# Performance work log

Measured on AMD Instinct MI355X. Metric: run time of the kernel, lower is better.

## Reference

```python
import jax, jax.numpy as jnp
import numpy as np

N = 50000
E = 800000
IN_C = 128
HID = 64
HEADS = 4
NUM_CLASSES = 10
NUM_GRAPHS = 64
EPS = 1e-5
NEG_SLOPE = 0.2


def setup_inputs() -> dict:
    key = jax.random.key(0)
    ks = jax.random.split(key, 32)
    inp = {}
    inp["x"] = jax.random.normal(ks[0], (N, IN_C), dtype=jnp.float32)
    inp["edge_index"] = jax.random.randint(ks[1], (2, E), 0, N, dtype=jnp.int32)
    inp["batch"] = jnp.sort(jax.random.randint(ks[2], (N,), 0, NUM_GRAPHS, dtype=jnp.int32))
    s = 0.05
    # GATConv1: in=128 -> heads=4, hid=64, concat -> 256
    inp["W1"] = jax.random.normal(ks[3], (IN_C, HEADS * HID), dtype=jnp.float32) * s
    inp["a_src1"] = jax.random.normal(ks[4], (HEADS, HID), dtype=jnp.float32) * s
    inp["a_dst1"] = jax.random.normal(ks[5], (HEADS, HID), dtype=jnp.float32) * s
    inp["b1"] = jnp.zeros((HEADS * HID,), dtype=jnp.float32)
    inp["g1"] = jnp.ones((HEADS * HID,), dtype=jnp.float32)
    inp["be1"] = jnp.zeros((HEADS * HID,), dtype=jnp.float32)
    # GATConv2: in=256 -> heads=4, hid=64, concat -> 256
    inp["W2"] = jax.random.normal(ks[6], (HEADS * HID, HEADS * HID), dtype=jnp.float32) * s
    inp["a_src2"] = jax.random.normal(ks[7], (HEADS, HID), dtype=jnp.float32) * s
    inp["a_dst2"] = jax.random.normal(ks[8], (HEADS, HID), dtype=jnp.float32) * s
    inp["b2"] = jnp.zeros((HEADS * HID,), dtype=jnp.float32)
    inp["g2"] = jnp.ones((HEADS * HID,), dtype=jnp.float32)
    inp["be2"] = jnp.zeros((HEADS * HID,), dtype=jnp.float32)
    # GATConv3: in=256 -> heads=1, hid=64, mean (concat=False) -> 64
    inp["W3"] = jax.random.normal(ks[9], (HEADS * HID, 1 * HID), dtype=jnp.float32) * s
    inp["a_src3"] = jax.random.normal(ks[10], (1, HID), dtype=jnp.float32) * s
    inp["a_dst3"] = jax.random.normal(ks[11], (1, HID), dtype=jnp.float32) * s
    inp["b3"] = jnp.zeros((HID,), dtype=jnp.float32)
    inp["g3"] = jnp.ones((HID,), dtype=jnp.float32)
    inp["be3"] = jnp.zeros((HID,), dtype=jnp.float32)
    # final classifier
    inp["fcW"] = jax.random.normal(ks[12], (HID, NUM_CLASSES), dtype=jnp.float32) * s
    inp["fcb"] = jnp.zeros((NUM_CLASSES,), dtype=jnp.float32)
    return inp


def gat_conv(x, src, dst, W, a_src, a_dst, b, heads, out_c, concat):
    # Linear transform, split heads: [N, H, C]
    h = (x @ W).reshape(-1, heads, out_c)
    # Per-node attention logits (dot with per-head attention vectors): [N, H]
    as_ = jnp.einsum("nhc,hc->nh", h, a_src)
    ad_ = jnp.einsum("nhc,hc->nh", h, a_dst)
    # Per-edge unnormalized attention (src contributes a_src, dst a_dst)
    e = jax.nn.leaky_relu(as_[src] + ad_[dst], NEG_SLOPE)  # [E, H]
    # Segment softmax over destination node (stable)
    e_max = jax.ops.segment_max(e, dst, num_segments=N)  # [N, H]
    ex = jnp.exp(e - e_max[dst])
    denom = jax.ops.segment_sum(ex, dst, num_segments=N)  # [N, H]
    alpha = ex / denom[dst]  # [E, H]
    # Weighted scatter-aggregate of source features
    msg = h[src] * alpha[:, :, None]  # [E, H, C]
    out = jax.ops.segment_sum(msg, dst, num_segments=N)  # [N, H, C]
    out = out.reshape(-1, heads * out_c) if concat else out.mean(axis=1)
    return out + b


def batch_norm(x, gamma, beta):
    mean = x.mean(axis=0)
    var = x.var(axis=0)
    return (x - mean) * jax.lax.rsqrt(var + EPS) * gamma + beta


def reference(x, edge_index, batch, W1, a_src1, a_dst1, b1, g1, be1,
              W2, a_src2, a_dst2, b2, g2, be2,
              W3, a_src3, a_dst3, b3, g3, be3, fcW, fcb):
    src, dst = edge_index[0], edge_index[1]
    h = jax.nn.relu(gat_conv(x, src, dst, W1, a_src1, a_dst1, b1, HEADS, HID, True))
    h = batch_norm(h, g1, be1)  # dropout = identity (eval)
    h = jax.nn.relu(gat_conv(h, src, dst, W2, a_src2, a_dst2, b2, HEADS, HID, True))
    h = batch_norm(h, g2, be2)
    h = jax.nn.relu(gat_conv(h, src, dst, W3, a_src3, a_dst3, b3, 1, HID, False))
    h = batch_norm(h, g3, be3)
    # global mean pool over graphs
    sums = jax.ops.segment_sum(h, batch, num_segments=NUM_GRAPHS)  # [G, HID]
    counts = jax.ops.segment_sum(jnp.ones((h.shape[0],), h.dtype), batch, num_segments=NUM_GRAPHS)
    pooled = sums / jnp.maximum(counts, 1.0)[:, None]
    return pooled @ fcW + fcb
```

## Files before the change

kernel.cpp:

```cpp
#include <hip/hip_runtime.h>
#include <hip/hip_bf16.h>

#define N_NODES 50000
#define NUM_E   800000
#define EPS_BN  1e-5f
#define NUM_GRAPHS 64

typedef __attribute__((ext_vector_type(8))) short bf16x8;
typedef __attribute__((ext_vector_type(4))) float f32x4;
typedef unsigned short ushort_t;
typedef unsigned int uint_t;

static __device__ __forceinline__ unsigned short f2bf(float f) {
    unsigned int u = __float_as_uint(f);
    u += 0x7fffu + ((u >> 16) & 1u);
    return (unsigned short)(u >> 16);
}
static __device__ __forceinline__ uint_t pkbf(float lo, float hi) {
    __hip_bfloat162 t = __float22bfloat162_rn(make_float2(lo, hi));
    return *(uint_t*)&t;
}
static __device__ __forceinline__ float bflo(uint_t u) { return __uint_as_float(u << 16); }
static __device__ __forceinline__ float bfhi(uint_t u) { return __uint_as_float(u & 0xffff0000u); }

__global__ void hist_kernel(const int* __restrict__ ei, int* __restrict__ deg) {
    int e = blockIdx.x * blockDim.x + threadIdx.x;
    if (e >= NUM_E) return;
    atomicAdd(&deg[ei[NUM_E + e]], 1);
}

__global__ void scan_local_kernel(const int* __restrict__ deg, int* __restrict__ rowptr,
                                  int* __restrict__ bsum) {
    __shared__ int ws[4];
    int b = blockIdx.x, t = threadIdx.x;
    int i = b * 256 + t;
    int lane = t & 63, wv = t >> 6;
    int v = (i < N_NODES) ? deg[i] : 0;
    int incl = v;
#pragma unroll
    for (int off = 1; off < 64; off <<= 1) {
        int u = __shfl_up(incl, off, 64);
        if (lane >= off) incl += u;
    }
    if (lane == 63) ws[wv] = incl;
    __syncthreads();
    if (t == 0) {
        int s = 0;
#pragma unroll
        for (int k = 0; k < 4; ++k) { int x = ws[k]; ws[k] = s; s += x; }
        bsum[b] = s;
    }
    __syncthreads();
    if (i < N_NODES) rowptr[i + 1] = ws[wv] + incl;
}

__global__ void scan_sums_kernel(int* __restrict__ bsum, int nb) {
    __shared__ int ws[4];
    int t = threadIdx.x;
    int lane = t & 63, wv = t >> 6;
    int v = (t < nb) ? bsum[t] : 0;
    int incl = v;
#pragma unroll
    for (int off = 1; off < 64; off <<= 1) {
        int u = __shfl_up(incl, off, 64);
        if (lane >= off) incl += u;
    }
    if (lane == 63) ws[wv] = incl;
    __syncthreads();
    if (t == 0) {
        int s = 0;
#pragma unroll
        for (int k = 0; k < 4; ++k) { int x = ws[k]; ws[k] = s; s += x; }
    }
    __syncthreads();
    if (t < nb) bsum[t] = ws[wv] + incl - v;
}

__global__ void scan_add_kernel(int* __restrict__ rowptr, const int* __restrict__ bsum) {
    int b = blockIdx.x, t = threadIdx.x;
    int i = b * 256 + t;
    if (i < N_NODES) rowptr[i + 1] += bsum[b];
    if (b == 0 && t == 0) rowptr[0] = 0;
}

__global__ void scatter_kernel(const int* __restrict__ ei, const int* __restrict__ rowptr,
                               int* __restrict__ fill, int* __restrict__ srcs) {
    int e = blockIdx.x * blockDim.x + threadIdx.x;
    if (e >= NUM_E) return;
    int dst = ei[NUM_E + e];
    int pos = rowptr[dst] + atomicAdd(&fill[dst], 1);
    srcs[pos] = ei[e];
}

__global__ void batch_offsets_kernel(const int* __restrict__ batch, int* __restrict__ goff) {
    int g = threadIdx.x;
    if (g > NUM_GRAPHS) return;
    int lo = 0, hi = N_NODES;
    while (lo < hi) {
        int mid = (lo + hi) >> 1;
        if (batch[mid] < g) lo = mid + 1; else hi = mid;
    }
    goff[g] = lo;
}

__global__ void prep_all_kernel(const float* __restrict__ W1, const float* __restrict__ W2,
                                const float* __restrict__ W3, const float* __restrict__ x,
                                ushort_t* __restrict__ w1t, ushort_t* __restrict__ w2t,
                                ushort_t* __restrict__ w3t, ushort_t* __restrict__ xbf) {
    const int S1 = 128 * 256, S2 = 256 * 256, S3 = 256 * 64;
    const int SW = S1 + S2 + S3;
    const int SX = N_NODES * 128 / 4;
    int i = blockIdx.x * blockDim.x + threadIdx.x;
    if (i < SX) {
        float4 v = ((const float4*)x)[i];
        ((uint2*)xbf)[i] = make_uint2(pkbf(v.x, v.y), pkbf(v.z, v.w));
    } else if (i < SX + SW) {
        int j = i - SX;
        if (j < S1) {
            int k = j / 256, n = j % 256;
            w1t[n * 128 + k] = f2bf(W1[j]);
        } else if (j < S1 + S2) {
            int jj = j - S1; int k = jj / 256, n = jj % 256;
            w2t[n * 256 + k] = f2bf(W2[jj]);
        } else {
            int jj = j - S1 - S2; int k = jj / 64, n = jj % 64;
            w3t[n * 256 + k] = f2bf(W3[jj]);
        }
    }
}

template<int K, int NFULL, int BN>
__global__ __launch_bounds__(256) void gemm_fused_kernel(const ushort_t* __restrict__ A,
                                                         const ushort_t* __restrict__ Bt,
                                                         ushort_t* __restrict__ C,
                                                         const float* __restrict__ stats,
                                                         const float* __restrict__ g,
                                                         const float* __restrict__ be,
                                                         const float* __restrict__ a_src,
                                                         const float* __restrict__ a_dst,
                                                         float* __restrict__ as_,
                                                         float* __restrict__ ad_) {
    const int NT = BN / 16;
    const int NG = BN / 64;
    constexpr int LOOP_BYTES = (128 * 40 + BN * 40) * 2;
    constexpr int EPI_BYTES  = 4 * 32 * 64 * 2;
    constexpr int SMEM_BYTES = LOOP_BYTES > EPI_BYTES ? LOOP_BYTES : EPI_BYTES;
    __shared__ __align__(16) unsigned char smem[SMEM_BYTES];
    ushort_t (*As)[40]     = (ushort_t (*)[40])smem;
    ushort_t (*Bs)[40]     = (ushort_t (*)[40])(smem + 128 * 40 * 2);
    ushort_t (*Cs)[32][64] = (ushort_t (*)[32][64])smem;
    __shared__ __align__(16) float aff_a[K], aff_b[K];
    __shared__ float asrc_s[BN], adst_s[BN];
    int tid = threadIdx.x;
    int lane = tid & 63, w = tid >> 6;
    int row0 = blockIdx.x * 128, col0 = blockIdx.y * BN;
    int m_l = lane & 15, q = lane >> 4;

    for (int c = tid; c < K; c += 256) {
        float a = 1.f, b = 0.f;
        if (stats) {
            float m = stats[c] * (1.f / N_NODES);
            float var = fmaxf(stats[256 + c] * (1.f / N_NODES) - m * m, 0.f);
            float rs = rsqrtf(var + EPS_BN) * g[c];
            a = rs; b = be[c] - m * rs;
        }
        aff_a[c] = a; aff_b[c] = b;
    }
    if (tid < BN) {
        asrc_s[tid] = a_src[col0 + tid];
        adst_s[tid] = a_dst[col0 + tid];
    }
    __syncthreads();

    f32x4 acc[2][NT];
#pragma unroll
    for (int r = 0; r < 2; ++r)
#pragma unroll
        for (int c = 0; c < NT; ++c) acc[r][c] = (f32x4){0.f, 0.f, 0.f, 0.f};

    int ar = tid >> 1, ako = (tid & 1) * 16;

    for (int k0 = 0; k0 < K; k0 += 32) {
        uint_t ow[8];
        int gr = row0 + ar;
        uint4 u0 = make_uint4(0, 0, 0, 0), u1 = make_uint4(0, 0, 0, 0);
        if (gr < N_NODES) {
            const ushort_t* ap = A + (long)gr * K + k0 + ako;
            u0 = *(const uint4*)ap;
            u1 = *(const uint4*)(ap + 8);
        }
        uint_t uu[8] = {u0.x, u0.y, u0.z, u0.w, u1.x, u1.y, u1.z, u1.w};
#pragma unroll
        for (int t = 0; t < 8; ++t) {
            int k = k0 + ako + t * 2;
            float lo = bflo(uu[t]) * aff_a[k] + aff_b[k];
            float hi = bfhi(uu[t]) * aff_a[k + 1] + aff_b[k + 1];
            ow[t] = pkbf(lo, hi);
        }
        if constexpr (BN == 128) {
            int br = tid >> 1, bko = (tid & 1) * 16;
            const ushort_t* bp = Bt + (long)(col0 + br) * K + k0 + bko;
            uint4 b0 = *(const uint4*)bp;
            uint4 b1 = *(const uint4*)(bp + 8);
            *(uint4*)&As[ar][ako] = make_uint4(ow[0], ow[1], ow[2], ow[3]);
            *(uint4*)&As[ar][ako + 8] = make_uint4(ow[4], ow[5], ow[6], ow[7]);
            *(uint4*)&Bs[br][bko] = b0;
            *(uint4*)&Bs[br][bko + 8] = b1;
        } else {
            int br = tid >> 2, bko = (tid & 3) * 8;
            uint4 bv = *(const uint4*)(Bt + (long)(col0 + br) * K + k0 + bko);
            *(uint4*)&As[ar][ako] = make_uint4(ow[0], ow[1], ow[2], ow[3]);
            *(uint4*)&As[ar][ako + 8] = make_uint4(ow[4], ow[5], ow[6], ow[7]);
            *(uint4*)&Bs[br][bko] = bv;
        }
        __syncthreads();

        bf16x8 af[2];
#pragma unroll
        for (int r = 0; r < 2; ++r)
            af[r] = *(const bf16x8*)&As[w * 32 + r * 16 + m_l][q * 8];
#pragma unroll
        for (int c = 0; c < NT; ++c) {
            bf16x8 bf = *(const bf16x8*)&Bs[c * 16 + m_l][q * 8];
#pragma unroll
            for (int r = 0; r < 2; ++r)
                acc[r][c] = __builtin_amdgcn_mfma_f32_16x16x32_bf16(af[r], bf, acc[r][c], 0, 0, 0);
        }
        __syncthreads();
    }

    const int H = NFULL / 64;
#pragma unroll
    for (int gblk = 0; gblk < NG; ++gblk) {
        int hidx = blockIdx.y * NG + gblk;
        int colg = col0 + gblk * 64;
#pragma unroll
        for (int r = 0; r < 2; ++r)
#pragma unroll
            for (int cc = 0; cc < 4; ++cc)
#pragma unroll
                for (int i = 0; i < 4; ++i)
                    Cs[w][r * 16 + q * 4 + i][cc * 16 + m_l] = f2bf(acc[r][gblk * 4 + cc][i]);
#pragma unroll
        for (int j = 0; j < 4; ++j) {
            int flat = j * 64 + lane;
            int lr = flat >> 3, chg = flat & 7;
            int gr = row0 + w * 32 + lr;
            uint4 u = *(uint4*)&Cs[w][lr][chg * 8];
            float f0 = bflo(u.x), f1 = bfhi(u.x), f2 = bflo(u.y), f3 = bfhi(u.y);
            float f4 = bflo(u.z), f5 = bfhi(u.z), f6 = bflo(u.w), f7 = bfhi(u.w);
            int cb = gblk * 64 + chg * 8;
            float s1 = f0 * asrc_s[cb] + f1 * asrc_s[cb + 1] + f2 * asrc_s[cb + 2] + f3 * asrc_s[cb + 3]
                     + f4 * asrc_s[cb + 4] + f5 * asrc_s[cb + 5] + f6 * asrc_s[cb + 6] + f7 * asrc_s[cb + 7];
            float s2 = f0 * adst_s[cb] + f1 * adst_s[cb + 1] + f2 * adst_s[cb + 2] + f3 * adst_s[cb + 3]
                     + f4 * adst_s[cb + 4] + f5 * adst_s[cb + 5] + f6 * adst_s[cb + 6] + f7 * adst_s[cb + 7];
#pragma unroll
            for (int o = 1; o < 8; o <<= 1) {
                s1 += __shfl_xor(s1, o, 64);
                s2 += __shfl_xor(s2, o, 64);
            }
            if (gr < N_NODES) {
                *(uint4*)(C + (long)gr * NFULL + colg + chg * 8) = u;
                if ((lane & 7) == 0) {
                    as_[gr * H + hidx] = s1;
                    ad_[gr * H + hidx] = s2;
                }
            }
        }
    }
}

__global__ __launch_bounds__(256) void agg4_kernel(const ushort_t* __restrict__ h,
                                                   const float* __restrict__ as_,
                                                   const float* __restrict__ ad_,
                                                   const int* __restrict__ rowptr,
                                                   const int* __restrict__ srcs,
                                                   const float* __restrict__ bias,
                                                   ushort_t* __restrict__ out) {
    __shared__ float4 alf[4][4][17];
    __shared__ int    sed[4][4][17];
    int tid = threadIdx.x;
    int lane = tid & 63, w = tid >> 6;
    int q = lane >> 4, cl = lane & 15;
    int n = blockIdx.x * 16 + w * 4 + q;

    int start = rowptr[n];
    int deg = rowptr[n + 1] - start;

    float4 adv = *(const float4*)(ad_ + n * 4);
    float ad4[4] = {adv.x, adv.y, adv.z, adv.w};

    float mx[4] = {-1e30f, -1e30f, -1e30f, -1e30f};
    float dn[4] = {0.f, 0.f, 0.f, 0.f};
    {
        float vst[4] = {-1e30f, -1e30f, -1e30f, -1e30f};
        int s0 = 0;
        if (deg > 0) s0 = srcs[start + min(cl, deg - 1)];
        sed[w][q][cl] = s0;
        if (cl < deg) {
            float4 av = *(const float4*)(as_ + s0 * 4);
            float vv[4] = {av.x + ad4[0], av.y + ad4[1], av.z + ad4[2], av.w + ad4[3]};
#pragma unroll
            for (int hh = 0; hh < 4; ++hh) {
                float v = vv[hh] > 0.f ? vv[hh] : 0.2f * vv[hh];
                vst[hh] = v; mx[hh] = v; dn[hh] = 1.f;
            }
        }
        alf[w][q][cl] = make_float4(vst[0], vst[1], vst[2], vst[3]);
        for (int j = cl + 16; j < deg; j += 16) {
            int s = srcs[start + j];
            float4 av = *(const float4*)(as_ + s * 4);
            float vv[4] = {av.x + ad4[0], av.y + ad4[1], av.z + ad4[2], av.w + ad4[3]};
#pragma unroll
            for (int hh = 0; hh < 4; ++hh) {
                float v = vv[hh] > 0.f ? vv[hh] : 0.2f * vv[hh];
                float mn = fmaxf(mx[hh], v);
                dn[hh] = dn[hh] * __expf(mx[hh] - mn) + __expf(v - mn);
                mx[hh] = mn;
            }
        }
    }
    float mloc[4] = {mx[0], mx[1], mx[2], mx[3]};
#pragma unroll
    for (int off = 1; off < 16; off <<= 1)
#pragma unroll
        for (int hh = 0; hh < 4; ++hh) mx[hh] = fmaxf(mx[hh], __shfl_xor(mx[hh], off, 64));
#pragma unroll
    for (int hh = 0; hh < 4; ++hh) dn[hh] *= __expf(mloc[hh] - mx[hh]);
#pragma unroll
    for (int off = 1; off < 16; off <<= 1)
#pragma unroll
        for (int hh = 0; hh < 4; ++hh) dn[hh] += __shfl_xor(dn[hh], off, 64);
    float inv[4];
#pragma unroll
    for (int hh = 0; hh < 4; ++hh) inv[hh] = dn[hh] > 0.f ? 1.f / dn[hh] : 0.f;
    {
        float4 vv = alf[w][q][cl];
        alf[w][q][cl] = make_float4(__expf(vv.x - mx[0]) * inv[0], __expf(vv.y - mx[1]) * inv[1],
                                    __expf(vv.z - mx[2]) * inv[2], __expf(vv.w - mx[3]) * inv[3]);
    }

    int hd = cl >> 2, cbase = cl * 16;
    float acc[16];
#pragma unroll
    for (int k = 0; k < 16; ++k) acc[k] = 0.f;

    for (int chunk = 0; chunk < deg || chunk == 0; chunk += 16) {
        if (chunk > 0) {
            int j = chunk + cl;
            int s = srcs[start + min(j, deg - 1)];
            sed[w][q][cl] = s;
            float a4[4] = {0.f, 0.f, 0.f, 0.f};
            if (j < deg) {
                float4 av = *(const float4*)(as_ + s * 4);
                float vv[4] = {av.x + ad4[0], av.y + ad4[1], av.z + ad4[2], av.w + ad4[3]};
#pragma unroll
                for (int hh = 0; hh < 4; ++hh) {
                    float v = vv[hh] > 0.f ? vv[hh] : 0.2f * vv[hh];
                    a4[hh] = __expf(v - mx[hh]) * inv[hh];
                }
            }
            alf[w][q][cl] = make_float4(a4[0], a4[1], a4[2], a4[3]);
        }
        int cnt = min(16, deg - chunk);
        if (cnt < 0) cnt = 0;
        int e = 0;
        for (; e + 4 <= cnt; e += 4) {
            float av[4]; int sv[4];
#pragma unroll
            for (int t = 0; t < 4; ++t) {
                av[t] = ((const float*)&alf[w][q][e + t])[hd];
                sv[t] = sed[w][q][e + t];
            }
            uint4 ua[4];
#pragma unroll
            for (int t = 0; t < 4; ++t)
                ua[t] = *(const uint4*)(h + (long)sv[t] * 256 + cbase);
#pragma unroll
            for (int t = 0; t < 4; ++t) {
                float al = av[t];
                acc[0] += al * bflo(ua[t].x); acc[1] += al * bfhi(ua[t].x);
                acc[2] += al * bflo(ua[t].y); acc[3] += al * bfhi(ua[t].y);
                acc[4] += al * bflo(ua[t].z); acc[5] += al * bfhi(ua[t].z);
                acc[6] += al * bflo(ua[t].w); acc[7] += al * bfhi(ua[t].w);
            }
#pragma unroll
            for (int t = 0; t < 4; ++t)
                ua[t] = *(const uint4*)(h + (long)sv[t] * 256 + cbase + 8);
#pragma unroll
            for (int t = 0; t < 4; ++t) {
                float al = av[t];
                acc[8]  += al * bflo(ua[t].x); acc[9]  += al * bfhi(ua[t].x);
                acc[10] += al * bflo(ua[t].y); acc[11] += al * bfhi(ua[t].y);
                acc[12] += al * bflo(ua[t].z); acc[13] += al * bfhi(ua[t].z);
                acc[14] += al * bflo(ua[t].w); acc[15] += al * bfhi(ua[t].w);
            }
        }
        for (; e < cnt; ++e) {
            float al = ((const float*)&alf[w][q][e])[hd];
            const ushort_t* hr = h + (long)sed[w][q][e] * 256 + cbase;
            uint4 u0 = *(const uint4*)hr;
            uint4 u1 = *(const uint4*)(hr + 8);
            acc[0]  += al * bflo(u0.x); acc[1]  += al * bfhi(u0.x);
            acc[2]  += al * bflo(u0.y); acc[3]  += al * bfhi(u0.y);
            acc[4]  += al * bflo(u0.z); acc[5]  += al * bfhi(u0.z);
            acc[6]  += al * bflo(u0.w); acc[7]  += al * bfhi(u0.w);
            acc[8]  += al * bflo(u1.x); acc[9]  += al * bfhi(u1.x);
            acc[10] += al * bflo(u1.y); acc[11] += al * bfhi(u1.y);
            acc[12] += al * bflo(u1.z); acc[13] += al * bfhi(u1.z);
            acc[14] += al * bflo(u1.w); acc[15] += al * bfhi(u1.w);
        }
        if (deg <= 16) break;
    }

    uint_t ow[8];
#pragma unroll
    for (int t = 0; t < 8; ++t) {
        float lo = fmaxf(acc[t * 2] + bias[cbase + t * 2], 0.f);
        float hi = fmaxf(acc[t * 2 + 1] + bias[cbase + t * 2 + 1], 0.f);
        ow[t] = pkbf(lo, hi);
    }
    ushort_t* op = out + (long)n * 256 + cbase;
    *(uint4*)op = make_uint4(ow[0], ow[1], ow[2], ow[3]);
    *(uint4*)(op + 8) = make_uint4(ow[4], ow[5], ow[6], ow[7]);
}

__global__ __launch_bounds__(256) void agg1_kernel(const ushort_t* __restrict__ h,
                                                   const float* __restrict__ as_,
                                                   const float* __restrict__ ad_,
                                                   const int* __restrict__ rowptr,
                                                   const int* __restrict__ srcs,
                                                   const float* __restrict__ bias,
                                                   ushort_t* __restrict__ out,
                                                   float* __restrict__ stats) {
    __shared__ float alf1[4][8][9];
    __shared__ int   sed1[4][8][9];
    __shared__ float ssum[64], ssq[64];
    int tid = threadIdx.x;
    int lane = tid & 63, w = tid >> 6;
    int o = lane >> 3, cl = lane & 7;
    int n = blockIdx.x * 32 + w * 8 + o;
    bool valid = n < N_NODES;
    int nc = valid ? n : N_NODES - 1;
    if (tid < 64) { ssum[tid] = 0.f; ssq[tid] = 0.f; }
    __syncthreads();

    int start = rowptr[nc];
    int deg = valid ? rowptr[nc + 1] - start : 0;
    float adn = ad_[nc];

    float mx = -1e30f, dn = 0.f;
    {
        float vst = -1e30f;
        int s0 = 0;
        if (deg > 0) s0 = srcs[start + min(cl, deg - 1)];
        sed1[w][o][cl] = s0;
        if (cl < deg) {
            float v = as_[s0] + adn;
            v = v > 0.f ? v : 0.2f * v;
            vst = v; mx = v; dn = 1.f;
        }
        alf1[w][o][cl] = vst;
        for (int j = cl + 8; j < deg; j += 8) {
            int s = srcs[start + j];
            float v = as_[s] + adn;
            v = v > 0.f ? v : 0.2f * v;
            float mn = fmaxf(mx, v);
            dn = dn * __expf(mx - mn) + __expf(v - mn);
            mx = mn;
        }
    }
    float mloc = mx;
#pragma unroll
    for (int off = 1; off < 8; off <<= 1) mx = fmaxf(mx, __shfl_xor(mx, off, 64));
    dn *= __expf(mloc - mx);
#pragma unroll
    for (int off = 1; off < 8; off <<= 1) dn += __shfl_xor(dn, off, 64);
    float inv = dn > 0.f ? 1.f / dn : 0.f;

    alf1[w][o][cl] = __expf(alf1[w][o][cl] - mx) * inv;

    int c0 = cl * 8;
    float acc[8] = {0.f, 0.f, 0.f, 0.f, 0.f, 0.f, 0.f, 0.f};

    for (int chunk = 0; chunk < deg || chunk == 0; chunk += 8) {
        if (chunk > 0) {
            int j = chunk + cl;
            int s = srcs[start + min(j, deg - 1)];
            sed1[w][o][cl] = s;
            float al = 0.f;
            if (j < deg) {
                float v = as_[s] + adn;
                v = v > 0.f ? v : 0.2f * v;
                al = __expf(v - mx) * inv;
            }
            alf1[w][o][cl] = al;
        }
        int cnt = min(8, deg - chunk);
        if (cnt < 0) cnt = 0;
        int e = 0;
        for (; e + 4 <= cnt; e += 4) {
            float av[4]; int sv[4];
#pragma unroll
            for (int t = 0; t < 4; ++t) {
                av[t] = alf1[w][o][e + t];
                sv[t] = sed1[w][o][e + t];
            }
            uint4 ua[4];
#pragma unroll
            for (int t = 0; t < 4; ++t)
                ua[t] = *(const uint4*)(h + (long)sv[t] * 64 + c0);
#pragma unroll
            for (int t = 0; t < 4; ++t) {
                float al = av[t];
                acc[0] += al * bflo(ua[t].x); acc[1] += al * bfhi(ua[t].x);
                acc[2] += al * bflo(ua[t].y); acc[3] += al * bfhi(ua[t].y);
                acc[4] += al * bflo(ua[t].z); acc[5] += al * bfhi(ua[t].z);
                acc[6] += al * bflo(ua[t].w); acc[7] += al * bfhi(ua[t].w);
            }
        }
        for (; e < cnt; ++e) {
            float al = alf1[w][o][e];
            uint4 u = *(const uint4*)(h + (long)sed1[w][o][e] * 64 + c0);
            acc[0] += al * bflo(u.x); acc[1] += al * bfhi(u.x);
            acc[2] += al * bflo(u.y); acc[3] += al * bfhi(u.y);
            acc[4] += al * bflo(u.z); acc[5] += al * bfhi(u.z);
            acc[6] += al * bflo(u.w); acc[7] += al * bfhi(u.w);
        }
        if (deg <= 8) break;
    }

    float v[8];
#pragma unroll
    for (int t = 0; t < 8; ++t) v[t] = fmaxf(acc[t] + bias[c0 + t], 0.f);
    if (valid) {
        uint_t ow[4];
#pragma unroll
        for (int t = 0; t < 4; ++t) ow[t] = pkbf(v[2 * t], v[2 * t + 1]);
        *(uint4*)(out + (long)n * 64 + c0) = make_uint4(ow[0], ow[1], ow[2], ow[3]);
    }
    float s1[8], s2[8];
#pragma unroll
    for (int t = 0; t < 8; ++t) {
        s1[t] = valid ? v[t] : 0.f;
        s2[t] = valid ? v[t] * v[t] : 0.f;
    }
#pragma unroll
    for (int off = 8; off < 64; off <<= 1)
#pragma unroll
        for (int t = 0; t < 8; ++t) {
            s1[t] += __shfl_xor(s1[t], off, 64);
            s2[t] += __shfl_xor(s2[t], off, 64);
        }
    if (lane < 8) {
#pragma unroll
        for (int t = 0; t < 8; ++t) {
            atomicAdd(&ssum[c0 + t], s1[t]);
            atomicAdd(&ssq[c0 + t], s2[t]);
        }
    }
    __syncthreads();
    if (tid < 64) {
        atomicAdd(&stats[tid], ssum[tid]);
        atomicAdd(&stats[256 + tid], ssq[tid]);
    }
}

template<int C>
__global__ __launch_bounds__(256) void bn_stats_bf16(const ushort_t* __restrict__ x,
                                                     float* __restrict__ stats) {
    const int GROUPS = C / 8;
    const int RS = 256 / GROUPS;
    int tid = threadIdx.x;
    int cg_ = tid % GROUPS;
    int rs = tid / GROUPS;
    float s[8], s2[8];
#pragma unroll
    for (int k = 0; k < 8; ++k) { s[k] = 0.f; s2[k] = 0.f; }
    for (int n = blockIdx.x * RS + rs; n < N_NODES; n += gridDim.x * RS) {
        uint4 u = *(const uint4*)(x + (long)n * C + cg_ * 8);
        float f[8] = {bflo(u.x), bfhi(u.x), bflo(u.y), bfhi(u.y),
                      bflo(u.z), bfhi(u.z), bflo(u.w), bfhi(u.w)};
#pragma unroll
        for (int k = 0; k < 8; ++k) { s[k] += f[k]; s2[k] += f[k] * f[k]; }
    }
    __shared__ float red[256][16];
#pragma unroll
    for (int k = 0; k < 8; ++k) { red[tid][k] = s[k]; red[tid][8 + k] = s2[k]; }
    __syncthreads();
    if (tid < C) {
        int g = tid >> 3, k = tid & 7;
        float a = 0.f, b = 0.f;
        for (int r = 0; r < RS; ++r) {
            a += red[g + r * GROUPS][k];
            b += red[g + r * GROUPS][8 + k];
        }
        atomicAdd(&stats[tid], a);
        atomicAdd(&stats[256 + tid], b);
    }
}

__global__ __launch_bounds__(256) void pool_fc_kernel(const ushort_t* __restrict__ h,
                                                      const int* __restrict__ goff,
                                                      const float* __restrict__ stats,
                                                      const float* __restrict__ g3,
                                                      const float* __restrict__ be3,
                                                      const float* __restrict__ fcW,
                                                      const float* __restrict__ fcb,
                                                      float* __restrict__ out) {
    int g = blockIdx.x;
    int c = threadIdx.x & 63;
    int ty = threadIdx.x >> 6;
    int s = goff[g], e = goff[g + 1];
    float sum = 0.f;
    for (int n = s + ty; n < e; n += 4) sum += bflo((uint_t)h[(long)n * 64 + c]);
    __shared__ float red[4][64];
    __shared__ float pv[64];
    red[ty][c] = sum;
    __syncthreads();
    if (ty == 0) {
        float tot = red[0][c] + red[1][c] + red[2][c] + red[3][c];
        float v = tot / fmaxf((float)(e - s), 1.f);
        float m = stats[c] * (1.f / N_NODES);
        float var = fmaxf(stats[256 + c] * (1.f / N_NODES) - m * m, 0.f);
        pv[c] = (v - m) * rsqrtf(var + EPS_BN) * g3[c] + be3[c];
    }
    __syncthreads();
    if (threadIdx.x < 10) {
        int j = threadIdx.x;
        float acc = fcb[j];
#pragma unroll
        for (int k = 0; k < 64; ++k) acc += pv[k] * fcW[k * 10 + j];
        out[g * 10 + j] = acc;
    }
}

extern "C" void kernel_launch(void* const* d_in, const int* in_sizes, int n_in,
                              void* d_out, int out_size, void* d_ws, size_t ws_size,
                              hipStream_t stream) {
    const float* x      = (const float*)d_in[0];
    const int*   ei     = (const int*)d_in[1];
    const int*   batch  = (const int*)d_in[2];
    const float* W1     = (const float*)d_in[3];
    const float* a_src1 = (const float*)d_in[4];
    const float* a_dst1 = (const float*)d_in[5];
    const float* b1     = (const float*)d_in[6];
    const float* g1     = (const float*)d_in[7];
    const float* be1    = (const float*)d_in[8];
    const float* W2     = (const float*)d_in[9];
    const float* a_src2 = (const float*)d_in[10];
    const float* a_dst2 = (const float*)d_in[11];
    const float* b2     = (const float*)d_in[12];
    const float* g2     = (const float*)d_in[13];
    const float* be2    = (const float*)d_in[14];
    const float* W3     = (const float*)d_in[15];
    const float* a_src3 = (const float*)d_in[16];
    const float* a_dst3 = (const float*)d_in[17];
    const float* b3     = (const float*)d_in[18];
    const float* g3     = (const float*)d_in[19];
    const float* be3    = (const float*)d_in[20];
    const float* fcW    = (const float*)d_in[21];
    const float* fcb    = (const float*)d_in[22];
    float* out = (float*)d_out;

    const size_t N = N_NODES, E = NUM_E;
    ushort_t* hbf    = (ushort_t*)d_ws;
    ushort_t* hagg   = hbf + N * 256;
    ushort_t* xbf    = hagg + N * 256;
    ushort_t* w1t    = xbf + N * 128;
    ushort_t* w2t    = w1t + 256 * 128;
    ushort_t* w3t    = w2t + 256 * 256;
    float*    as_    = (float*)(w3t + 64 * 256 + 128);
    float*    ad_    = as_ + N * 4;
    int*      deg    = (int*)(ad_ + N * 4);
    int*      fill   = deg + N;
    float*    statsA = (float*)(fill + N);
    float*    statsB = statsA + 512;
    float*    statsC = statsB + 512;
    int*      rowptr = (int*)(statsC + 512);
    int*      srcs   = rowptr + (N + 1);
    int*      bsum   = srcs + E;
    int*      goff   = bsum + 256;

    const int NB = (N_NODES + 255) / 256;

    hipMemsetAsync(deg, 0, sizeof(int) * (2 * N + 3 * 512), stream);
    hist_kernel<<<(NUM_E + 255) / 256, 256, 0, stream>>>(ei, deg);
    scan_local_kernel<<<NB, 256, 0, stream>>>(deg, rowptr, bsum);
    scan_sums_kernel<<<1, 256, 0, stream>>>(bsum, NB);
    scan_add_kernel<<<NB, 256, 0, stream>>>(rowptr, bsum);
    scatter_kernel<<<(NUM_E + 255) / 256, 256, 0, stream>>>(ei, rowptr, fill, srcs);
    batch_offsets_kernel<<<1, 128, 0, stream>>>(batch, goff);
    prep_all_kernel<<<(N_NODES * 128 / 4 + 128 * 256 + 256 * 256 + 256 * 64 + 255) / 256, 256, 0, stream>>>(
        W1, W2, W3, x, w1t, w2t, w3t, xbf);

    const int GB = (N_NODES + 127) / 128;
    const int AB = N_NODES / 16;

    gemm_fused_kernel<128, 256, 128><<<dim3(GB, 2), 256, 0, stream>>>(
        xbf, w1t, hbf, nullptr, nullptr, nullptr, a_src1, a_dst1, as_, ad_);
    agg4_kernel<<<AB, 256, 0, stream>>>(hbf, as_, ad_, rowptr, srcs, b1, hagg);
    bn_stats_bf16<256><<<128, 256, 0, stream>>>(hagg, statsA);

    gemm_fused_kernel<256, 256, 128><<<dim3(GB, 2), 256, 0, stream>>>(
        hagg, w2t, hbf, statsA, g1, be1, a_src2, a_dst2, as_, ad_);
    agg4_kernel<<<AB, 256, 0, stream>>>(hbf, as_, ad_, rowptr, srcs, b2, hagg);
    bn_stats_bf16<256><<<128, 256, 0, stream>>>(hagg, statsB);

    gemm_fused_kernel<256, 64, 64><<<dim3(GB, 1), 256, 0, stream>>>(
        hagg, w3t, hbf, statsB, g2, be2, a_src3, a_dst3, as_, ad_);
    agg1_kernel<<<(N_NODES + 31) / 32, 256, 0, stream>>>(hbf, as_, ad_, rowptr, srcs, b3, hagg, statsC);

    pool_fc_kernel<<<NUM_GRAPHS, 256, 0, stream>>>(hagg, goff, statsC, g3, be3, fcW, fcb, out);
}
```

Before: 525.1 us.

## Fold batch-norm affine into GEMM weights and epilogue bias vector

Rather than applying the batch-norm scale and shift to every A element inside the GEMM load loop, a small kernel pre-scales the transposed weights by the per-channel scale and computes a per-output-column bias (shift times W). The GEMM then stages raw A tiles straight into shared memory and adds the bias in the epilogue. This removes per-element unpack, FMA and repack work from the main loop, at the cost of two extra small kernel launches and a different bf16 rounding point (scaled weights are rounded instead of normalized activations).

```diff
diff --git a/kernel.cpp b/kernel.cpp
--- a/kernel.cpp
+++ b/kernel.cpp
@@ -129,13 +129,34 @@
     }
 }
 
+__global__ __launch_bounds__(256) void scale_w_kernel(const float* __restrict__ stats,
+                                                      const float* __restrict__ g,
+                                                      const float* __restrict__ be,
+                                                      const ushort_t* __restrict__ wt,
+                                                      ushort_t* __restrict__ wts,
+                                                      float* __restrict__ cvec) {
+    int n = blockIdx.x, k = threadIdx.x;
+    float m = stats[k] * (1.f / N_NODES);
+    float var = fmaxf(stats[256 + k] * (1.f / N_NODES) - m * m, 0.f);
+    float rs = rsqrtf(var + EPS_BN) * g[k];
+    float b = be[k] - m * rs;
+    float wv = bflo((uint_t)wt[n * 256 + k]);
+    wts[n * 256 + k] = f2bf(rs * wv);
+    float p = b * wv;
+    __shared__ float ws[4];
+    int lane = k & 63, wid = k >> 6;
+#pragma unroll
+    for (int off = 1; off < 64; off <<= 1) p += __shfl_xor(p, off, 64);
+    if (lane == 0) ws[wid] = p;
+    __syncthreads();
+    if (k == 0) cvec[n] = ws[0] + ws[1] + ws[2] + ws[3];
+}
+
 template<int K, int NFULL, int BN>
 __global__ __launch_bounds__(256) void gemm_fused_kernel(const ushort_t* __restrict__ A,
                                                          const ushort_t* __restrict__ Bt,
                                                          ushort_t* __restrict__ C,
-                                                         const float* __restrict__ stats,
-                                                         const float* __restrict__ g,
-                                                         const float* __restrict__ be,
+                                                         const float* __restrict__ cvec,
                                                          const float* __restrict__ a_src,
                                                          const float* __restrict__ a_dst,
                                                          float* __restrict__ as_,
@@ -149,24 +170,15 @@
     ushort_t (*As)[40]     = (ushort_t (*)[40])smem;
     ushort_t (*Bs)[40]     = (ushort_t (*)[40])(smem + 128 * 40 * 2);
     ushort_t (*Cs)[32][64] = (ushort_t (*)[32][64])smem;
-    __shared__ __align__(16) float aff_a[K], aff_b[K];
+    __shared__ float cvec_s[BN];
     __shared__ float asrc_s[BN], adst_s[BN];
     int tid = threadIdx.x;
     int lane = tid & 63, w = tid >> 6;
     int row0 = blockIdx.x * 128, col0 = blockIdx.y * BN;
     int m_l = lane & 15, q = lane >> 4;
 
-    for (int c = tid; c < K; c += 256) {
-        float a = 1.f, b = 0.f;
-        if (stats) {
-            float m = stats[c] * (1.f / N_NODES);
-            float var = fmaxf(stats[256 + c] * (1.f / N_NODES) - m * m, 0.f);
-            float rs = rsqrtf(var + EPS_BN) * g[c];
-            a = rs; b = be[c] - m * rs;
-        }
-        aff_a[c] = a; aff_b[c] = b;
-    }
     if (tid < BN) {
+        cvec_s[tid] = cvec[col0 + tid];
         asrc_s[tid] = a_src[col0 + tid];
         adst_s[tid] = a_dst[col0 + tid];
     }
@@ -181,7 +193,6 @@
     int ar = tid >> 1, ako = (tid & 1) * 16;
 
     for (int k0 = 0; k0 < K; k0 += 32) {
-        uint_t ow[8];
         int gr = row0 + ar;
         uint4 u0 = make_uint4(0, 0, 0, 0), u1 = make_uint4(0, 0, 0, 0);
         if (gr < N_NODES) {
@@ -189,28 +200,20 @@
             u0 = *(const uint4*)ap;
             u1 = *(const uint4*)(ap + 8);
         }
-        uint_t uu[8] = {u0.x, u0.y, u0.z, u0.w, u1.x, u1.y, u1.z, u1.w};
-#pragma unroll
-        for (int t = 0; t < 8; ++t) {
-            int k = k0 + ako + t * 2;
-            float lo = bflo(uu[t]) * aff_a[k] + aff_b[k];
-            float hi = bfhi(uu[t]) * aff_a[k + 1] + aff_b[k + 1];
-            ow[t] = pkbf(lo, hi);
-        }
         if constexpr (BN == 128) {
             int br = tid >> 1, bko = (tid & 1) * 16;
             const ushort_t* bp = Bt + (long)(col0 + br) * K + k0 + bko;
             uint4 b0 = *(const uint4*)bp;
             uint4 b1 = *(const uint4*)(bp + 8);
-            *(uint4*)&As[ar][ako] = make_uint4(ow[0], ow[1], ow[2], ow[3]);
-            *(uint4*)&As[ar][ako + 8] = make_uint4(ow[4], ow[5], ow[6], ow[7]);
+            *(uint4*)&As[ar][ako] = u0;
+            *(uint4*)&As[ar][ako + 8] = u1;
             *(uint4*)&Bs[br][bko] = b0;
             *(uint4*)&Bs[br][bko + 8] = b1;
         } else {
             int br = tid >> 2, bko = (tid & 3) * 8;
             uint4 bv = *(const uint4*)(Bt + (long)(col0 + br) * K + k0 + bko);
-            *(uint4*)&As[ar][ako] = make_uint4(ow[0], ow[1], ow[2], ow[3]);
-            *(uint4*)&As[ar][ako + 8] = make_uint4(ow[4], ow[5], ow[6], ow[7]);
+            *(uint4*)&As[ar][ako] = u0;
+            *(uint4*)&As[ar][ako + 8] = u1;
             *(uint4*)&Bs[br][bko] = bv;
         }
         __syncthreads();
@@ -240,7 +243,8 @@
             for (int cc = 0; cc < 4; ++cc)
 #pragma unroll
                 for (int i = 0; i < 4; ++i)
-                    Cs[w][r * 16 + q * 4 + i][cc * 16 + m_l] = f2bf(acc[r][gblk * 4 + cc][i]);
+                    Cs[w][r * 16 + q * 4 + i][cc * 16 + m_l] =
+                        f2bf(acc[r][gblk * 4 + cc][i] + cvec_s[gblk * 64 + cc * 16 + m_l]);
 #pragma unroll
         for (int j = 0; j < 4; ++j) {
             int flat = j * 64 + lane;
@@ -670,21 +674,26 @@
     ushort_t* w1t    = xbf + N * 128;
     ushort_t* w2t    = w1t + 256 * 128;
     ushort_t* w3t    = w2t + 256 * 256;
-    float*    as_    = (float*)(w3t + 64 * 256 + 128);
+    ushort_t* w2ts   = w3t + 64 * 256;
+    ushort_t* w3ts   = w2ts + 256 * 256;
+    float*    as_    = (float*)(w3ts + 64 * 256 + 128);
     float*    ad_    = as_ + N * 4;
     int*      deg    = (int*)(ad_ + N * 4);
     int*      fill   = deg + N;
     float*    statsA = (float*)(fill + N);
     float*    statsB = statsA + 512;
     float*    statsC = statsB + 512;
-    int*      rowptr = (int*)(statsC + 512);
+    float*    cvec0  = statsC + 512;
+    int*      rowptr = (int*)(cvec0 + 256);
     int*      srcs   = rowptr + (N + 1);
     int*      bsum   = srcs + E;
     int*      goff   = bsum + 256;
+    float*    cvec2  = (float*)(goff + 72);
+    float*    cvec3  = cvec2 + 256;
 
     const int NB = (N_NODES + 255) / 256;
 
-    hipMemsetAsync(deg, 0, sizeof(int) * (2 * N + 3 * 512), stream);
+    hipMemsetAsync(deg, 0, sizeof(int) * (2 * N + 3 * 512 + 256), stream);
     hist_kernel<<<(NUM_E + 255) / 256, 256, 0, stream>>>(ei, deg);
     scan_local_kernel<<<NB, 256, 0, stream>>>(deg, rowptr, bsum);
     scan_sums_kernel<<<1, 256, 0, stream>>>(bsum, NB);
@@ -698,17 +707,19 @@
     const int AB = N_NODES / 16;
 
     gemm_fused_kernel<128, 256, 128><<<dim3(GB, 2), 256, 0, stream>>>(
-        xbf, w1t, hbf, nullptr, nullptr, nullptr, a_src1, a_dst1, as_, ad_);
+        xbf, w1t, hbf, cvec0, a_src1, a_dst1, as_, ad_);
     agg4_kernel<<<AB, 256, 0, stream>>>(hbf, as_, ad_, rowptr, srcs, b1, hagg);
     bn_stats_bf16<256><<<128, 256, 0, stream>>>(hagg, statsA);
 
+    scale_w_kernel<<<256, 256, 0, stream>>>(statsA, g1, be1, w2t, w2ts, cvec2);
     gemm_fused_kernel<256, 256, 128><<<dim3(GB, 2), 256, 0, stream>>>(
-        hagg, w2t, hbf, statsA, g1, be1, a_src2, a_dst2, as_, ad_);
+        hagg, w2ts, hbf, cvec2, a_src2, a_dst2, as_, ad_);
     agg4_kernel<<<AB, 256, 0, stream>>>(hbf, as_, ad_, rowptr, srcs, b2, hagg);
     bn_stats_bf16<256><<<128, 256, 0, stream>>>(hagg, statsB);
 
+    scale_w_kernel<<<64, 256, 0, stream>>>(statsB, g2, be2, w3t, w3ts, cvec3);
     gemm_fused_kernel<256, 64, 64><<<dim3(GB, 1), 256, 0, stream>>>(
-        hagg, w3t, hbf, statsB, g2, be2, a_src3, a_dst3, as_, ad_);
+        hagg, w3ts, hbf, cvec3, a_src3, a_dst3, as_, ad_);
     agg1_kernel<<<(N_NODES + 31) / 32, 256, 0, stream>>>(hbf, as_, ad_, rowptr, srcs, b3, hagg, statsC);
 
     pool_fc_kernel<<<NUM_GRAPHS, 256, 0, stream>>>(hagg, goff, statsC, g3, be3, fcW, fcb, out);
```

After: 523.5 us. No clear change (-0.3%).

## Fuse preprocessing kernels, merge scatter into first GEMM, spread BN stat atomics

Applied to the files above, without the earlier changes.

Merges the degree histogram with the weight/input bf16 conversion into one launch, and folds the two-level scan fixup into a single kernel that reduces the block sums itself. The CSR scatter now runs as extra blocks inside the first GEMM launch, and the graph offset search moves into the pool kernel. BN statistics atomics are spread over 64 copies to reduce contention, and readers sum the copies. The aim is fewer launches and serialized small kernels, at the cost of a larger memset and redundant prefix sums in every fixup block.

```diff
diff --git a/kernel.cpp b/kernel.cpp
--- a/kernel.cpp
+++ b/kernel.cpp
@@ -5,6 +5,7 @@
 #define NUM_E   800000
 #define EPS_BN  1e-5f
 #define NUM_GRAPHS 64
+#define NCOPY 64
 
 typedef __attribute__((ext_vector_type(8))) short bf16x8;
 typedef __attribute__((ext_vector_type(4))) float f32x4;
@@ -23,94 +24,22 @@
 static __device__ __forceinline__ float bflo(uint_t u) { return __uint_as_float(u << 16); }
 static __device__ __forceinline__ float bfhi(uint_t u) { return __uint_as_float(u & 0xffff0000u); }
 
-__global__ void hist_kernel(const int* __restrict__ ei, int* __restrict__ deg) {
-    int e = blockIdx.x * blockDim.x + threadIdx.x;
-    if (e >= NUM_E) return;
-    atomicAdd(&deg[ei[NUM_E + e]], 1);
-}
-
-__global__ void scan_local_kernel(const int* __restrict__ deg, int* __restrict__ rowptr,
-                                  int* __restrict__ bsum) {
-    __shared__ int ws[4];
-    int b = blockIdx.x, t = threadIdx.x;
-    int i = b * 256 + t;
-    int lane = t & 63, wv = t >> 6;
-    int v = (i < N_NODES) ? deg[i] : 0;
-    int incl = v;
-#pragma unroll
-    for (int off = 1; off < 64; off <<= 1) {
-        int u = __shfl_up(incl, off, 64);
-        if (lane >= off) incl += u;
-    }
-    if (lane == 63) ws[wv] = incl;
-    __syncthreads();
-    if (t == 0) {
-        int s = 0;
-#pragma unroll
-        for (int k = 0; k < 4; ++k) { int x = ws[k]; ws[k] = s; s += x; }
-        bsum[b] = s;
-    }
-    __syncthreads();
-    if (i < N_NODES) rowptr[i + 1] = ws[wv] + incl;
-}
-
-__global__ void scan_sums_kernel(int* __restrict__ bsum, int nb) {
-    __shared__ int ws[4];
-    int t = threadIdx.x;
-    int lane = t & 63, wv = t >> 6;
-    int v = (t < nb) ? bsum[t] : 0;
-    int incl = v;
-#pragma unroll
-    for (int off = 1; off < 64; off <<= 1) {
-        int u = __shfl_up(incl, off, 64);
-        if (lane >= off) incl += u;
-    }
-    if (lane == 63) ws[wv] = incl;
-    __syncthreads();
-    if (t == 0) {
-        int s = 0;
-#pragma unroll
-        for (int k = 0; k < 4; ++k) { int x = ws[k]; ws[k] = s; s += x; }
-    }
-    __syncthreads();
-    if (t < nb) bsum[t] = ws[wv] + incl - v;
-}
-
-__global__ void scan_add_kernel(int* __restrict__ rowptr, const int* __restrict__ bsum) {
-    int b = blockIdx.x, t = threadIdx.x;
-    int i = b * 256 + t;
-    if (i < N_NODES) rowptr[i + 1] += bsum[b];
-    if (b == 0 && t == 0) rowptr[0] = 0;
-}
-
-__global__ void scatter_kernel(const int* __restrict__ ei, const int* __restrict__ rowptr,
-                               int* __restrict__ fill, int* __restrict__ srcs) {
-    int e = blockIdx.x * blockDim.x + threadIdx.x;
-    if (e >= NUM_E) return;
-    int dst = ei[NUM_E + e];
-    int pos = rowptr[dst] + atomicAdd(&fill[dst], 1);
-    srcs[pos] = ei[e];
-}
-
-__global__ void batch_offsets_kernel(const int* __restrict__ batch, int* __restrict__ goff) {
-    int g = threadIdx.x;
-    if (g > NUM_GRAPHS) return;
-    int lo = 0, hi = N_NODES;
-    while (lo < hi) {
-        int mid = (lo + hi) >> 1;
-        if (batch[mid] < g) lo = mid + 1; else hi = mid;
-    }
-    goff[g] = lo;
-}
-
-__global__ void prep_all_kernel(const float* __restrict__ W1, const float* __restrict__ W2,
-                                const float* __restrict__ W3, const float* __restrict__ x,
-                                ushort_t* __restrict__ w1t, ushort_t* __restrict__ w2t,
-                                ushort_t* __restrict__ w3t, ushort_t* __restrict__ xbf) {
+__global__ void hist_prep_kernel(const int* __restrict__ ei, int* __restrict__ deg,
+                                 const float* __restrict__ W1, const float* __restrict__ W2,
+                                 const float* __restrict__ W3, const float* __restrict__ x,
+                                 ushort_t* __restrict__ w1t, ushort_t* __restrict__ w2t,
+                                 ushort_t* __restrict__ w3t, ushort_t* __restrict__ xbf) {
+    const int HB = (NUM_E + 255) / 256;
     const int S1 = 128 * 256, S2 = 256 * 256, S3 = 256 * 64;
     const int SW = S1 + S2 + S3;
     const int SX = N_NODES * 128 / 4;
-    int i = blockIdx.x * blockDim.x + threadIdx.x;
+    int b = blockIdx.x;
+    if (b < HB) {
+        int e = b * 256 + threadIdx.x;
+        if (e < NUM_E) atomicAdd(&deg[ei[NUM_E + e]], 1);
+        return;
+    }
+    int i = (b - HB) * 256 + threadIdx.x;
     if (i < SX) {
         float4 v = ((const float4*)x)[i];
         ((uint2*)xbf)[i] = make_uint2(pkbf(v.x, v.y), pkbf(v.z, v.w));
@@ -129,7 +58,48 @@
     }
 }
 
-template<int K, int NFULL, int BN>
+__global__ void scan_local_kernel(const int* __restrict__ deg, int* __restrict__ rowptr,
+                                  int* __restrict__ bsum) {
+    __shared__ int ws[4];
+    int b = blockIdx.x, t = threadIdx.x;
+    int i = b * 256 + t;
+    int lane = t & 63, wv = t >> 6;
+    int v = (i < N_NODES) ? deg[i] : 0;
+    int incl = v;
+#pragma unroll
+    for (int off = 1; off < 64; off <<= 1) {
+        int u = __shfl_up(incl, off, 64);
+        if (lane >= off) incl += u;
+    }
+    if (lane == 63) ws[wv] = incl;
+    __syncthreads();
+    if (t == 0) {
+        int s = 0;
+#pragma unroll
+        for (int k = 0; k < 4; ++k) { int x = ws[k]; ws[k] = s; s += x; }
+        bsum[b] = s;
+    }
+    __syncthreads();
+    if (i < N_NODES) rowptr[i + 1] = ws[wv] + incl;
+}
+
+__global__ __launch_bounds__(256) void scan_fixup_kernel(int* __restrict__ rowptr,
+                                                         const int* __restrict__ bsum) {
+    __shared__ int ws[4];
+    int b = blockIdx.x, t = threadIdx.x;
+    int lane = t & 63, wv = t >> 6;
+    int v = (t < b) ? bsum[t] : 0;
+#pragma unroll
+    for (int off = 1; off < 64; off <<= 1) v += __shfl_xor(v, off, 64);
+    if (lane == 0) ws[wv] = v;
+    __syncthreads();
+    int pre = ws[0] + ws[1] + ws[2] + ws[3];
+    int i = b * 256 + t;
+    if (i < N_NODES) rowptr[i + 1] += pre;
+    if (b == 0 && t == 0) rowptr[0] = 0;
+}
+
+template<int K, int NFULL, int BN, bool SCAT>
 __global__ __launch_bounds__(256) void gemm_fused_kernel(const ushort_t* __restrict__ A,
                                                          const ushort_t* __restrict__ Bt,
                                                          ushort_t* __restrict__ C,
@@ -139,7 +109,24 @@
                                                          const float* __restrict__ a_src,
                                                          const float* __restrict__ a_dst,
                                                          float* __restrict__ as_,
-                                                         float* __restrict__ ad_) {
+                                                         float* __restrict__ ad_,
+                                                         const int* __restrict__ ei,
+                                                         const int* __restrict__ rowptr,
+                                                         int* __restrict__ fill,
+                                                         int* __restrict__ srcs) {
+    constexpr int GBX = (N_NODES + 127) / 128;
+    if constexpr (SCAT) {
+        if (blockIdx.x >= GBX) {
+            int idx = (blockIdx.x - GBX) + 1563 * blockIdx.y;
+            int e = idx * 256 + (int)threadIdx.x;
+            if (e < NUM_E) {
+                int dst = ei[NUM_E + e];
+                int pos = rowptr[dst] + atomicAdd(&fill[dst], 1);
+                srcs[pos] = ei[e];
+            }
+            return;
+        }
+    }
     const int NT = BN / 16;
     const int NG = BN / 64;
     constexpr int LOOP_BYTES = (128 * 40 + BN * 40) * 2;
@@ -159,8 +146,14 @@
     for (int c = tid; c < K; c += 256) {
         float a = 1.f, b = 0.f;
         if (stats) {
-            float m = stats[c] * (1.f / N_NODES);
-            float var = fmaxf(stats[256 + c] * (1.f / N_NODES) - m * m, 0.f);
+            float s0 = 0.f, s1 = 0.f;
+#pragma unroll 8
+            for (int j = 0; j < NCOPY; ++j) {
+                s0 += stats[j * 512 + c];
+                s1 += stats[j * 512 + 256 + c];
+            }
+            float m = s0 * (1.f / N_NODES);
+            float var = fmaxf(s1 * (1.f / N_NODES) - m * m, 0.f);
             float rs = rsqrtf(var + EPS_BN) * g[c];
             a = rs; b = be[c] - m * rs;
         }
@@ -561,8 +554,9 @@
     }
     __syncthreads();
     if (tid < 64) {
-        atomicAdd(&stats[tid], ssum[tid]);
-        atomicAdd(&stats[256 + tid], ssq[tid]);
+        int cp = (blockIdx.x & (NCOPY - 1)) * 512;
+        atomicAdd(&stats[cp + tid], ssum[tid]);
+        atomicAdd(&stats[cp + 256 + tid], ssq[tid]);
     }
 }
 
@@ -595,13 +589,14 @@
             a += red[g + r * GROUPS][k];
             b += red[g + r * GROUPS][8 + k];
         }
-        atomicAdd(&stats[tid], a);
-        atomicAdd(&stats[256 + tid], b);
+        int cp = (blockIdx.x & (NCOPY - 1)) * 512;
+        atomicAdd(&stats[cp + tid], a);
+        atomicAdd(&stats[cp + 256 + tid], b);
     }
 }
 
 __global__ __launch_bounds__(256) void pool_fc_kernel(const ushort_t* __restrict__ h,
-                                                      const int* __restrict__ goff,
+                                                      const int* __restrict__ batch,
                                                       const float* __restrict__ stats,
                                                       const float* __restrict__ g3,
                                                       const float* __restrict__ be3,
@@ -609,9 +604,20 @@
                                                       const float* __restrict__ fcb,
                                                       float* __restrict__ out) {
     int g = blockIdx.x;
+    __shared__ int se[2];
+    if (threadIdx.x < 2) {
+        int gg = g + threadIdx.x;
+        int lo = 0, hi = N_NODES;
+        while (lo < hi) {
+            int mid = (lo + hi) >> 1;
+            if (batch[mid] < gg) lo = mid + 1; else hi = mid;
+        }
+        se[threadIdx.x] = lo;
+    }
+    __syncthreads();
+    int s = se[0], e = se[1];
     int c = threadIdx.x & 63;
     int ty = threadIdx.x >> 6;
-    int s = goff[g], e = goff[g + 1];
     float sum = 0.f;
     for (int n = s + ty; n < e; n += 4) sum += bflo((uint_t)h[(long)n * 64 + c]);
     __shared__ float red[4][64];
@@ -621,8 +627,14 @@
     if (ty == 0) {
         float tot = red[0][c] + red[1][c] + red[2][c] + red[3][c];
         float v = tot / fmaxf((float)(e - s), 1.f);
-        float m = stats[c] * (1.f / N_NODES);
-        float var = fmaxf(stats[256 + c] * (1.f / N_NODES) - m * m, 0.f);
+        float s0 = 0.f, s1 = 0.f;
+#pragma unroll 8
+        for (int j = 0; j < NCOPY; ++j) {
+            s0 += stats[j * 512 + c];
+            s1 += stats[j * 512 + 256 + c];
+        }
+        float m = s0 * (1.f / N_NODES);
+        float var = fmaxf(s1 * (1.f / N_NODES) - m * m, 0.f);
         pv[c] = (v - m) * rsqrtf(var + EPS_BN) * g3[c] + be3[c];
     }
     __syncthreads();
@@ -664,6 +676,7 @@
     float* out = (float*)d_out;
 
     const size_t N = N_NODES, E = NUM_E;
+    const int SST = NCOPY * 512;
     ushort_t* hbf    = (ushort_t*)d_ws;
     ushort_t* hagg   = hbf + N * 256;
     ushort_t* xbf    = hagg + N * 256;
@@ -675,41 +688,42 @@
     int*      deg    = (int*)(ad_ + N * 4);
     int*      fill   = deg + N;
     float*    statsA = (float*)(fill + N);
-    float*    statsB = statsA + 512;
-    float*    statsC = statsB + 512;
-    int*      rowptr = (int*)(statsC + 512);
+    float*    statsB = statsA + SST;
+    float*    statsC = statsB + SST;
+    int*      rowptr = (int*)(statsC + SST);
     int*      srcs   = rowptr + (N + 1);
     int*      bsum   = srcs + E;
-    int*      goff   = bsum + 256;
 
     const int NB = (N_NODES + 255) / 256;
-
-    hipMemsetAsync(deg, 0, sizeof(int) * (2 * N + 3 * 512), stream);
-    hist_kernel<<<(NUM_E + 255) / 256, 256, 0, stream>>>(ei, deg);
+    const int HB = (NUM_E + 255) / 256;
+    const int SX = N_NODES * 128 / 4;
+    const int SW = 128 * 256 + 256 * 256 + 256 * 64;
+    const int PB = (SX + SW + 255) / 256;
+
+    hipMemsetAsync(deg, 0, sizeof(int) * (2 * N + 3 * SST), stream);
+    hist_prep_kernel<<<HB + PB, 256, 0, stream>>>(ei, deg, W1, W2, W3, x, w1t, w2t, w3t, xbf);
     scan_local_kernel<<<NB, 256, 0, stream>>>(deg, rowptr, bsum);
-    scan_sums_kernel<<<1, 256, 0, stream>>>(bsum, NB);
-    scan_add_kernel<<<NB, 256, 0, stream>>>(rowptr, bsum);
-    scatter_kernel<<<(NUM_E + 255) / 256, 256, 0, stream>>>(ei, rowptr, fill, srcs);
-    batch_offsets_kernel<<<1, 128, 0, stream>>>(batch, goff);
-    prep_all_kernel<<<(N_NODES * 128 / 4 + 128 * 256 + 256 * 256 + 256 * 64 + 255) / 256, 256, 0, stream>>>(
-        W1, W2, W3, x, w1t, w2t, w3t, xbf);
+    scan_fixup_kernel<<<NB, 256, 0, stream>>>(rowptr, bsum);
 
     const int GB = (N_NODES + 127) / 128;
     const int AB = N_NODES / 16;
 
-    gemm_fused_kernel<128, 256, 128><<<dim3(GB, 2), 256, 0, stream>>>(
-        xbf, w1t, hbf, nullptr, nullptr, nullptr, a_src1, a_dst1, as_, ad_);
+    gemm_fused_kernel<128, 256, 128, true><<<dim3(GB + 1563, 2), 256, 0, stream>>>(
+        xbf, w1t, hbf, nullptr, nullptr, nullptr, a_src1, a_dst1, as_, ad_,
+        ei, rowptr, fill, srcs);
     agg4_kernel<<<AB, 256, 0, stream>>>(hbf, as_, ad_, rowptr, srcs, b1, hagg);
     bn_stats_bf16<256><<<128, 256, 0, stream>>>(hagg, statsA);
 
-    gemm_fused_kernel<256, 256, 128><<<dim3(GB, 2), 256, 0, stream>>>(
-        hagg, w2t, hbf, statsA, g1, be1, a_src2, a_dst2, as_, ad_);
+    gemm_fused_kernel<256, 256, 128, false><<<dim3(GB, 2), 256, 0, stream>>>(
+        hagg, w2t, hbf, statsA, g1, be1, a_src2, a_dst2, as_, ad_,
+        nullptr, nullptr, nullptr, nullptr);
     agg4_kernel<<<AB, 256, 0, stream>>>(hbf, as_, ad_, rowptr, srcs, b2, hagg);
     bn_stats_bf16<256><<<128, 256, 0, stream>>>(hagg, statsB);
 
-    gemm_fused_kernel<256, 64, 64><<<dim3(GB, 1), 256, 0, stream>>>(
-        hagg, w3t, hbf, statsB, g2, be2, a_src3, a_dst3, as_, ad_);
+    gemm_fused_kernel<256, 64, 64, false><<<dim3(GB, 1), 256, 0, stream>>>(
+        hagg, w3t, hbf, statsB, g2, be2, a_src3, a_dst3, as_, ad_,
+        nullptr, nullptr, nullptr, nullptr);
     agg1_kernel<<<(N_NODES + 31) / 32, 256, 0, stream>>>(hbf, as_, ad_, rowptr, srcs, b3, hagg, statsC);
 
-    pool_fc_kernel<<<NUM_GRAPHS, 256, 0, stream>>>(hagg, goff, statsC, g3, be3, fcW, fcb, out);
-}
+    pool_fc_kernel<<<NUM_GRAPHS, 256, 0, stream>>>(hagg, batch, statsC, g3, be3, fcW, fcb, out);
+}
```

New measurement: 499.8 us. 1.05x faster.
